# Kernel optimization log

Measured on AMD Instinct MI355X. Metric: run time of the kernel, lower is better.

## Reference

```python
import jax
import jax.numpy as jnp
import numpy as np
from jax import lax

# D dags, L topological levels, K nodes per level, P predecessors per node,
# F = atom/hidden feature dim (104 in original), C = num classes (500)
D, L, K, P, F, C = 256, 64, 64, 8, 104, 500


def setup_inputs() -> dict:
    key = jax.random.key(0)
    ks = jax.random.split(key, 10)
    atom_feats = jax.random.normal(ks[0], (D, L, K, F), dtype=jnp.float32)
    pred_idx = jax.random.randint(ks[1], (D, L - 1, K, P), 0, K, dtype=jnp.int32)
    W1 = jax.random.normal(ks[2], (F, F), dtype=jnp.float32) * 0.1
    b1 = jnp.zeros((F,), dtype=jnp.float32)
    Wm = jax.random.normal(ks[3], (2 * F, F), dtype=jnp.float32) * 0.1
    bm = jnp.zeros((F,), dtype=jnp.float32)
    att_w = jax.random.uniform(ks[4], (F,), dtype=jnp.float32)  # torch.rand init
    dag_w = jax.random.uniform(ks[5], (F,), dtype=jnp.float32)
    Wf = jax.random.normal(ks[6], (F, C), dtype=jnp.float32) * 0.1
    bf = jnp.zeros((C,), dtype=jnp.float32)
    return {"atom_feats": atom_feats, "pred_idx": pred_idx, "W1": W1, "b1": b1,
            "Wm": Wm, "bm": bm, "att_w": att_w, "dag_w": dag_w, "Wf": Wf, "bf": bf}


def reference(atom_feats, pred_idx, W1, b1, Wm, bm, att_w, dag_w, Wf, bf):
    # Level 0: source nodes -> ReLU(NN_single_node(atom))
    out0 = jax.nn.relu(atom_feats[:, 0] @ W1 + b1)  # [D, K, F]

    def step(prev, xs):
        atoms, idx = xs  # atoms [D,K,F], idx [D,K,P]
        # gather predecessor outputs from previous topological level
        preds = jax.vmap(lambda p, i: p[i])(prev, idx)  # [D,K,P,F]
        # softmax attention over the predecessor (stack) axis, elementwise in F
        attn = jax.nn.softmax(att_w * preds, axis=2)
        agg = jnp.sum(attn * preds, axis=2)  # [D,K,F]
        # cat((aggregated, atom)) -> merge -> ReLU
        out = jax.nn.relu(jnp.concatenate([agg, atoms], axis=-1) @ Wm + bm)
        return out, None

    xs = (jnp.swapaxes(atom_feats[:, 1:], 0, 1),  # [L-1, D, K, F]
          jnp.swapaxes(pred_idx, 0, 1))           # [L-1, D, K, P]
    last, _ = lax.scan(step, out0, xs)
    # 'last' output per DAG = last node in topological order
    sink = last[:, -1]  # [D, F]
    # softmax attention over DAG axis with dag_weight, then final linear
    dag_attn = jax.nn.softmax(dag_w * sink, axis=0)
    pooled = jnp.sum(dag_attn * sink, axis=0)  # [F]
    return pooled @ Wf + bf  # [C]
```

## Files before the change

### kernel.cpp

```cpp
#include <hip/hip_runtime.h>
#include <cstddef>

#define Dn 256
#define Ln 64
#define Kn 64
#define Pn 8
#define Fn 104
#define Cn 500
#define KF 6656
#define TPB 896
#define PSTR 108
#define XROWB 512
#define NQ 1664

typedef __attribute__((ext_vector_type(8))) short bh8;
typedef __attribute__((ext_vector_type(4))) float f32x4;

__device__ __forceinline__ unsigned short f2bf_rne(float x) {
  unsigned u = __builtin_bit_cast(unsigned, x);
  u = (u + 0x7fffu + ((u >> 16) & 1u)) >> 16;
  return (unsigned short)u;
}
__device__ __forceinline__ float bf2f(unsigned short h) {
  unsigned u = ((unsigned)h) << 16;
  return __builtin_bit_cast(float, u);
}
__device__ __forceinline__ unsigned pkhi(float a, float b) {
  return __builtin_amdgcn_perm(__builtin_bit_cast(unsigned, b),
                               __builtin_bit_cast(unsigned, a), 0x07060302u);
}
__device__ __forceinline__ float hi_of(float x) {
  return __builtin_bit_cast(float, __builtin_bit_cast(unsigned, x) & 0xffff0000u);
}

__device__ __forceinline__ void stage_quad(char* XAc, char* XBc, int k, int c0,
                                           float v0, float v1, float v2, float v3) {
  uint2 hv, lv;
  hv.x = pkhi(v0, v1); hv.y = pkhi(v2, v3);
  const float r0 = v0 - hi_of(v0), r1 = v1 - hi_of(v1);
  const float r2 = v2 - hi_of(v2), r3 = v3 - hi_of(v3);
  lv.x = pkhi(r0, r1); lv.y = pkhi(r2, r3);
  const int off = k * XROWB + ((((c0 >> 3) ^ (k & 7)) << 4) | ((c0 & 7) << 1));
  *reinterpret_cast<uint2*>(XAc + off) = hv;
  *reinterpret_cast<uint2*>(XBc + off) = lv;
}

__device__ __forceinline__ void load_w_frags(const float* __restrict__ Wg, int Krows,
                                             int col, int e, bh8* Wh, bh8* Wl) {
  #pragma unroll
  for (int kt = 0; kt < 7; ++kt) {
    bh8 h, l;
    #pragma unroll
    for (int v = 0; v < 8; ++v) {
      int k = kt * 32 + e * 8 + v;
      float x = (k < Krows && col < Fn) ? Wg[k * Fn + col] : 0.f;
      unsigned short hh = f2bf_rne(x);
      unsigned short ll = f2bf_rne(x - bf2f(hh));
      h[v] = (short)hh; l[v] = (short)ll;
    }
    Wh[kt] = h; Wl[kt] = l;
  }
}

__device__ __forceinline__ void mfma_gemm(const char* XAc, const char* XBc,
                                          const bh8* Wh, const bh8* Wl,
                                          const float* bms, float* PREVs,
                                          int lane, int col, int mh) {
  const int e = lane >> 4;
  const int rb = lane & 15;
  const float bias = (col < Fn) ? bms[col] : 0.f;
  f32x4 acc[2];
  #pragma unroll
  for (int mti = 0; mti < 2; ++mti) { f32x4 b4 = {bias, bias, bias, bias}; acc[mti] = b4; }
  #pragma unroll
  for (int kt = 0; kt < 7; ++kt) {
    #pragma unroll
    for (int mti = 0; mti < 2; ++mti) {
      const int r = (mh * 2 + mti) * 16 + rb;
      const int chunk = (kt * 4 + e) ^ (rb & 7);
      const bh8 ah = *reinterpret_cast<const bh8*>(XAc + r * XROWB + chunk * 16);
      const bh8 al = *reinterpret_cast<const bh8*>(XBc + r * XROWB + chunk * 16);
      acc[mti] = __builtin_amdgcn_mfma_f32_16x16x32_bf16(ah, Wh[kt], acc[mti], 0, 0, 0);
      acc[mti] = __builtin_amdgcn_mfma_f32_16x16x32_bf16(al, Wh[kt], acc[mti], 0, 0, 0);
      acc[mti] = __builtin_amdgcn_mfma_f32_16x16x32_bf16(ah, Wl[kt], acc[mti], 0, 0, 0);
      acc[mti] = __builtin_amdgcn_mfma_f32_16x16x32_bf16(al, Wl[kt], acc[mti], 0, 0, 0);
    }
  }
  if (col < Fn) {
    #pragma unroll
    for (int mti = 0; mti < 2; ++mti) {
      #pragma unroll
      for (int j = 0; j < 4; ++j) {
        int r = (mh * 2 + mti) * 16 + e * 4 + j;
        PREVs[r * PSTR + col] = fmaxf(acc[mti][j], 0.f);
      }
    }
  }
}

__global__ __launch_bounds__(TPB) void scan_kernel(
    const float* __restrict__ af,
    const int*   __restrict__ pidx,
    const float* __restrict__ W1, const float* __restrict__ b1,
    const float* __restrict__ Wm, const float* __restrict__ bm,
    const float* __restrict__ att_w,
    float* __restrict__ sink)
{
  extern __shared__ char smem[];
  char*  XAc   = smem;
  char*  XBc   = smem + 32768;
  float* PREVs = (float*)(smem + 65536);
  float* bms   = (float*)(smem + 65536 + 27648);
  float* aws   = (float*)(smem + 65536 + 27648 + 448);
  int*   idxs  = (int*)  (smem + 65536 + 27648 + 448 + 416);

  const int t = threadIdx.x;
  const int d = blockIdx.x;
  const int lane = t & 63;
  const int wv = t >> 6;
  const int nt = wv % 7;
  const int mh = wv / 7;
  const int e = lane >> 4;
  const int col = nt * 16 + (lane & 15);

  const float*  afd = af + (size_t)d * (Ln * KF);
  const float4* af4 = reinterpret_cast<const float4*>(afd);
  const int*    pid = pidx + (size_t)d * ((Ln - 1) * Kn * Pn);

  bh8 Wh[7], Wl[7];
  float4 pf4[2];
  int ir0 = 0;

  for (int i = t; i < 16384; i += TPB) reinterpret_cast<unsigned*>(XAc)[i] = 0u;
  if (t < Fn) { bms[t] = b1[t]; aws[t] = att_w[t]; }
  else if (t < 112) bms[t] = 0.f;
  load_w_frags(W1, Fn, col, e, Wh, Wl);
  #pragma unroll
  for (int j = 0; j < 2; ++j) {
    int q = t + j * TPB;
    if (q < NQ) {
      int k = q / 26, fq = (q - k * 26) << 2;
      float4 v = af4[q];
      stage_quad(XAc, XBc, k, fq, v.x, v.y, v.z, v.w);
    }
  }
  __syncthreads();

  mfma_gemm(XAc, XBc, Wh, Wl, bms, PREVs, lane, col, mh);
  __syncthreads();

  load_w_frags(Wm, 2 * Fn, col, e, Wh, Wl);
  if (t < Fn) bms[t] = bm[t];
  if (t < 512) idxs[t] = pid[t];
  #pragma unroll
  for (int j = 0; j < 2; ++j) {
    int q = t + j * TPB;
    if (q < NQ) pf4[j] = af4[NQ + q];
  }
  __syncthreads();

  for (int l = 1; l < Ln; ++l) {
    #pragma unroll
    for (int j = 0; j < 2; ++j) {
      int q = t + j * TPB;
      if (q < NQ) {
        int k = q / 26, fq = (q - k * 26) << 2;
        float4 v = pf4[j];
        stage_quad(XAc, XBc, k, Fn + fq, v.x, v.y, v.z, v.w);
      }
    }
    if (l < 63) {
      const float4* an = af4 + (size_t)(l + 1) * NQ;
      #pragma unroll
      for (int j = 0; j < 2; ++j) {
        int q = t + j * TPB;
        if (q < NQ) pf4[j] = an[q];
      }
      if (t < 512) ir0 = pid[(size_t)l * 512 + t];
    }
    for (int q = t; q < NQ; q += TPB) {
      int k = q / 26, fq = (q - k * 26) << 2;
      const float4 w4 = *reinterpret_cast<const float4*>(aws + fq);
      const float wa[4] = {w4.x, w4.y, w4.z, w4.w};
      const int4 ia = *reinterpret_cast<const int4*>(idxs + (k << 3));
      const int4 ib = *reinterpret_cast<const int4*>(idxs + (k << 3) + 4);
      const int ip[8] = {ia.x, ia.y, ia.z, ia.w, ib.x, ib.y, ib.z, ib.w};
      float vv[8][4];
      #pragma unroll
      for (int p = 0; p < Pn; ++p) {
        float4 v4 = *reinterpret_cast<const float4*>(PREVs + ip[p] * PSTR + fq);
        vv[p][0] = v4.x; vv[p][1] = v4.y; vv[p][2] = v4.z; vv[p][3] = v4.w;
      }
      float ag[4];
      #pragma unroll
      for (int c = 0; c < 4; ++c) {
        float vmax = vv[0][c];
        #pragma unroll
        for (int p = 1; p < Pn; ++p) vmax = fmaxf(vmax, vv[p][c]);
        const float m = wa[c] * vmax;
        float es = 0.f, ps = 0.f;
        #pragma unroll
        for (int p = 0; p < Pn; ++p) {
          float ex = __expf(fmaf(wa[c], vv[p][c], -m));
          es += ex; ps += ex * vv[p][c];
        }
        ag[c] = ps * __builtin_amdgcn_rcpf(es);
      }
      stage_quad(XAc, XBc, k, fq, ag[0], ag[1], ag[2], ag[3]);
    }
    __syncthreads();

    mfma_gemm(XAc, XBc, Wh, Wl, bms, PREVs, lane, col, mh);
    if (l < 63 && t < 512) idxs[t] = ir0;
    __syncthreads();
  }

  if (t < Fn) sink[d * Fn + t] = PREVs[(Kn - 1) * PSTR + t];
}

__global__ __launch_bounds__(512) void final_kernel(
    const float* __restrict__ sink, const float* __restrict__ dag_w,
    const float* __restrict__ Wf, const float* __restrict__ bf,
    float* __restrict__ out)
{
  extern __shared__ char smem[];
  float* ss = (float*)smem;
  float* pooled = ss + Dn * Fn;
  const int t = threadIdx.x;
  for (int i = t; i < Dn * Fn; i += 512) ss[i] = sink[i];
  __syncthreads();
  if (t < Fn) {
    float wvv = dag_w[t];
    float m = -3.0e38f;
    for (int dd = 0; dd < Dn; ++dd) m = fmaxf(m, wvv * ss[dd * Fn + t]);
    float es = 0.f, ps = 0.f;
    for (int dd = 0; dd < Dn; ++dd) {
      float v = ss[dd * Fn + t];
      float ex = __expf(wvv * v - m);
      es += ex; ps += ex * v;
    }
    pooled[t] = ps / es;
  }
  __syncthreads();
  if (t < Cn) {
    float a = bf[t];
    for (int f = 0; f < Fn; ++f) a = fmaf(pooled[f], Wf[f * Cn + t], a);
    out[t] = a;
  }
}

extern "C" void kernel_launch(void* const* d_in, const int* in_sizes, int n_in,
                              void* d_out, int out_size, void* d_ws, size_t ws_size,
                              hipStream_t stream) {
  const float* af    = (const float*)d_in[0];
  const int*   pidx  = (const int*)  d_in[1];
  const float* W1    = (const float*)d_in[2];
  const float* b1    = (const float*)d_in[3];
  const float* Wm    = (const float*)d_in[4];
  const float* bm    = (const float*)d_in[5];
  const float* att_w = (const float*)d_in[6];
  const float* dag_w = (const float*)d_in[7];
  const float* Wf    = (const float*)d_in[8];
  const float* bf    = (const float*)d_in[9];
  float* out  = (float*)d_out;
  float* sink = (float*)d_ws;

  constexpr size_t SMEM1 = 96096;
  constexpr size_t SMEM2 = (size_t)(Dn * Fn + Fn) * 4;

  (void)hipFuncSetAttribute((const void*)scan_kernel,
                      hipFuncAttributeMaxDynamicSharedMemorySize, (int)SMEM1);
  (void)hipFuncSetAttribute((const void*)final_kernel,
                      hipFuncAttributeMaxDynamicSharedMemorySize, (int)SMEM2);

  scan_kernel<<<Dn, TPB, SMEM1, stream>>>(af, pidx, W1, b1, Wm, bm, att_w, sink);
  final_kernel<<<1, 512, SMEM2, stream>>>(sink, dag_w, Wf, bf, out);
}
```

Before: 364.3 us.

## Overlap atom-half GEMM with attention aggregation and trim split-bf16 MFMAs

Swaps the concat order so atom features occupy the first K-tiles, letting the atom part of the merge GEMM run before the predecessor softmax aggregation and only the aggregated part runs after the barrier. Drops the lo*lo MFMA term of the split-bf16 emulation, cutting a quarter of MFMA work at some accuracy cost. Softmax uses exp2 with att_w pre-scaled by log2(e), and packed f32 FMA/add/mul for the elementwise math. Adds an extra barrier per level and keeps the accumulators live across the aggregation phase, which raises register pressure.

```diff
diff --git a/kernel.cpp b/kernel.cpp
--- a/kernel.cpp
+++ b/kernel.cpp
@@ -1,5 +1,6 @@
 #include <hip/hip_runtime.h>
 #include <cstddef>
+#include <math.h>
 
 #define Dn 256
 #define Ln 64
@@ -15,6 +16,19 @@
 
 typedef __attribute__((ext_vector_type(8))) short bh8;
 typedef __attribute__((ext_vector_type(4))) float f32x4;
+typedef __attribute__((ext_vector_type(2))) float f32x2;
+
+__device__ __forceinline__ f32x2 pk_fma(f32x2 a, f32x2 b, f32x2 c) {
+  f32x2 d;
+  asm("v_pk_fma_f32 %0, %1, %2, %3" : "=v"(d) : "v"(a), "v"(b), "v"(c));
+  return d;
+}
+__device__ __forceinline__ f32x2 pk_add(f32x2 a, f32x2 b) {
+  f32x2 d; asm("v_pk_add_f32 %0, %1, %2" : "=v"(d) : "v"(a), "v"(b)); return d;
+}
+__device__ __forceinline__ f32x2 pk_mul(f32x2 a, f32x2 b) {
+  f32x2 d; asm("v_pk_mul_f32 %0, %1, %2" : "=v"(d) : "v"(a), "v"(b)); return d;
+}
 
 __device__ __forceinline__ unsigned short f2bf_rne(float x) {
   unsigned u = __builtin_bit_cast(unsigned, x);
@@ -62,18 +76,33 @@
   }
 }
 
-__device__ __forceinline__ void mfma_gemm(const char* XAc, const char* XBc,
+__device__ __forceinline__ void load_w_frags_swapped(const float* __restrict__ Wg,
+                                                     int col, int e, bh8* Wh, bh8* Wl) {
+  #pragma unroll
+  for (int kt = 0; kt < 7; ++kt) {
+    bh8 h, l;
+    #pragma unroll
+    for (int v = 0; v < 8; ++v) {
+      int k = kt * 32 + e * 8 + v;
+      int row = (k < Fn) ? (k + Fn) : (k < 2 * Fn ? k - Fn : -1);
+      float x = (row >= 0 && col < Fn) ? Wg[row * Fn + col] : 0.f;
+      unsigned short hh = f2bf_rne(x);
+      unsigned short ll = f2bf_rne(x - bf2f(hh));
+      h[v] = (short)hh; l[v] = (short)ll;
+    }
+    Wh[kt] = h; Wl[kt] = l;
+  }
+}
+
+__device__ __forceinline__ void gemm_part(const char* XAc, const char* XBc,
                                           const bh8* Wh, const bh8* Wl,
-                                          const float* bms, float* PREVs,
-                                          int lane, int col, int mh) {
+                                          f32x4 acc[2], int lane, int mh,
+                                          int k0, int k1) {
   const int e = lane >> 4;
   const int rb = lane & 15;
-  const float bias = (col < Fn) ? bms[col] : 0.f;
-  f32x4 acc[2];
-  #pragma unroll
-  for (int mti = 0; mti < 2; ++mti) { f32x4 b4 = {bias, bias, bias, bias}; acc[mti] = b4; }
   #pragma unroll
   for (int kt = 0; kt < 7; ++kt) {
+    if (kt < k0 || kt >= k1) continue;
     #pragma unroll
     for (int mti = 0; mti < 2; ++mti) {
       const int r = (mh * 2 + mti) * 16 + rb;
@@ -83,9 +112,13 @@
       acc[mti] = __builtin_amdgcn_mfma_f32_16x16x32_bf16(ah, Wh[kt], acc[mti], 0, 0, 0);
       acc[mti] = __builtin_amdgcn_mfma_f32_16x16x32_bf16(al, Wh[kt], acc[mti], 0, 0, 0);
       acc[mti] = __builtin_amdgcn_mfma_f32_16x16x32_bf16(ah, Wl[kt], acc[mti], 0, 0, 0);
-      acc[mti] = __builtin_amdgcn_mfma_f32_16x16x32_bf16(al, Wl[kt], acc[mti], 0, 0, 0);
-    }
-  }
+    }
+  }
+}
+
+__device__ __forceinline__ void gemm_epilogue(f32x4 acc[2], float* PREVs,
+                                              int lane, int col, int mh) {
+  const int e = lane >> 4;
   if (col < Fn) {
     #pragma unroll
     for (int mti = 0; mti < 2; ++mti) {
@@ -117,9 +150,9 @@
   const int t = threadIdx.x;
   const int d = blockIdx.x;
   const int lane = t & 63;
-  const int wv = t >> 6;
-  const int nt = wv % 7;
-  const int mh = wv / 7;
+  const int wvi = t >> 6;
+  const int nt = wvi % 7;
+  const int mh = wvi / 7;
   const int e = lane >> 4;
   const int col = nt * 16 + (lane & 15);
 
@@ -132,7 +165,7 @@
   int ir0 = 0;
 
   for (int i = t; i < 16384; i += TPB) reinterpret_cast<unsigned*>(XAc)[i] = 0u;
-  if (t < Fn) { bms[t] = b1[t]; aws[t] = att_w[t]; }
+  if (t < Fn) { bms[t] = b1[t]; aws[t] = att_w[t] * 1.44269504f; }
   else if (t < 112) bms[t] = 0.f;
   load_w_frags(W1, Fn, col, e, Wh, Wl);
   #pragma unroll
@@ -146,10 +179,17 @@
   }
   __syncthreads();
 
-  mfma_gemm(XAc, XBc, Wh, Wl, bms, PREVs, lane, col, mh);
-  __syncthreads();
-
-  load_w_frags(Wm, 2 * Fn, col, e, Wh, Wl);
+  {
+    const float bias = (col < Fn) ? bms[col] : 0.f;
+    f32x4 acc[2];
+    #pragma unroll
+    for (int mti = 0; mti < 2; ++mti) { f32x4 b4 = {bias, bias, bias, bias}; acc[mti] = b4; }
+    gemm_part(XAc, XBc, Wh, Wl, acc, lane, mh, 0, 4);
+    gemm_epilogue(acc, PREVs, lane, col, mh);
+  }
+  __syncthreads();
+
+  load_w_frags_swapped(Wm, col, e, Wh, Wl);
   if (t < Fn) bms[t] = bm[t];
   if (t < 512) idxs[t] = pid[t];
   #pragma unroll
@@ -166,7 +206,7 @@
       if (q < NQ) {
         int k = q / 26, fq = (q - k * 26) << 2;
         float4 v = pf4[j];
-        stage_quad(XAc, XBc, k, Fn + fq, v.x, v.y, v.z, v.w);
+        stage_quad(XAc, XBc, k, fq, v.x, v.y, v.z, v.w);
       }
     }
     if (l < 63) {
@@ -178,39 +218,66 @@
       }
       if (t < 512) ir0 = pid[(size_t)l * 512 + t];
     }
+    __syncthreads();
+
+    const float bias = (col < Fn) ? bms[col] : 0.f;
+    f32x4 acc[2];
+    #pragma unroll
+    for (int mti = 0; mti < 2; ++mti) { f32x4 b4 = {bias, bias, bias, bias}; acc[mti] = b4; }
+    gemm_part(XAc, XBc, Wh, Wl, acc, lane, mh, 0, 3);
+
     for (int q = t; q < NQ; q += TPB) {
       int k = q / 26, fq = (q - k * 26) << 2;
       const float4 w4 = *reinterpret_cast<const float4*>(aws + fq);
-      const float wa[4] = {w4.x, w4.y, w4.z, w4.w};
+      const f32x2 wa01 = {w4.x, w4.y}, wa23 = {w4.z, w4.w};
       const int4 ia = *reinterpret_cast<const int4*>(idxs + (k << 3));
       const int4 ib = *reinterpret_cast<const int4*>(idxs + (k << 3) + 4);
       const int ip[8] = {ia.x, ia.y, ia.z, ia.w, ib.x, ib.y, ib.z, ib.w};
-      float vv[8][4];
+      float4 vvp[8];
+      #pragma unroll
+      for (int p = 0; p < Pn; ++p)
+        vvp[p] = *reinterpret_cast<const float4*>(PREVs + ip[p] * PSTR + fq);
+      float m0, m1, m2, m3;
+      m0 = fmaxf(fmaxf(vvp[0].x, vvp[1].x), vvp[2].x);
+      m0 = fmaxf(fmaxf(m0, vvp[3].x), vvp[4].x);
+      m0 = fmaxf(fmaxf(m0, vvp[5].x), vvp[6].x);
+      m0 = fmaxf(m0, vvp[7].x);
+      m1 = fmaxf(fmaxf(vvp[0].y, vvp[1].y), vvp[2].y);
+      m1 = fmaxf(fmaxf(m1, vvp[3].y), vvp[4].y);
+      m1 = fmaxf(fmaxf(m1, vvp[5].y), vvp[6].y);
+      m1 = fmaxf(m1, vvp[7].y);
+      m2 = fmaxf(fmaxf(vvp[0].z, vvp[1].z), vvp[2].z);
+      m2 = fmaxf(fmaxf(m2, vvp[3].z), vvp[4].z);
+      m2 = fmaxf(fmaxf(m2, vvp[5].z), vvp[6].z);
+      m2 = fmaxf(m2, vvp[7].z);
+      m3 = fmaxf(fmaxf(vvp[0].w, vvp[1].w), vvp[2].w);
+      m3 = fmaxf(fmaxf(m3, vvp[3].w), vvp[4].w);
+      m3 = fmaxf(fmaxf(m3, vvp[5].w), vvp[6].w);
+      m3 = fmaxf(m3, vvp[7].w);
+      const f32x2 mm01 = {-m0, -m1}, mm23 = {-m2, -m3};
+      const f32x2 nm01 = pk_mul(wa01, mm01), nm23 = pk_mul(wa23, mm23);
+      f32x2 es01 = {0.f, 0.f}, es23 = {0.f, 0.f};
+      f32x2 ps01 = {0.f, 0.f}, ps23 = {0.f, 0.f};
       #pragma unroll
       for (int p = 0; p < Pn; ++p) {
-        float4 v4 = *reinterpret_cast<const float4*>(PREVs + ip[p] * PSTR + fq);
-        vv[p][0] = v4.x; vv[p][1] = v4.y; vv[p][2] = v4.z; vv[p][3] = v4.w;
+        const f32x2 v01 = {vvp[p].x, vvp[p].y}, v23 = {vvp[p].z, vvp[p].w};
+        const f32x2 a01 = pk_fma(wa01, v01, nm01);
+        const f32x2 a23 = pk_fma(wa23, v23, nm23);
+        const f32x2 e01 = {exp2f(a01.x), exp2f(a01.y)};
+        const f32x2 e23 = {exp2f(a23.x), exp2f(a23.y)};
+        es01 = pk_add(es01, e01); es23 = pk_add(es23, e23);
+        ps01 = pk_fma(e01, v01, ps01); ps23 = pk_fma(e23, v23, ps23);
       }
-      float ag[4];
-      #pragma unroll
-      for (int c = 0; c < 4; ++c) {
-        float vmax = vv[0][c];
-        #pragma unroll
-        for (int p = 1; p < Pn; ++p) vmax = fmaxf(vmax, vv[p][c]);
-        const float m = wa[c] * vmax;
-        float es = 0.f, ps = 0.f;
-        #pragma unroll
-        for (int p = 0; p < Pn; ++p) {
-          float ex = __expf(fmaf(wa[c], vv[p][c], -m));
-          es += ex; ps += ex * vv[p][c];
-        }
-        ag[c] = ps * __builtin_amdgcn_rcpf(es);
-      }
-      stage_quad(XAc, XBc, k, fq, ag[0], ag[1], ag[2], ag[3]);
+      const float ag0 = ps01.x * __builtin_amdgcn_rcpf(es01.x);
+      const float ag1 = ps01.y * __builtin_amdgcn_rcpf(es01.y);
+      const float ag2 = ps23.x * __builtin_amdgcn_rcpf(es23.x);
+      const float ag3 = ps23.y * __builtin_amdgcn_rcpf(es23.y);
+      stage_quad(XAc, XBc, k, Fn + fq, ag0, ag1, ag2, ag3);
     }
     __syncthreads();
 
-    mfma_gemm(XAc, XBc, Wh, Wl, bms, PREVs, lane, col, mh);
+    gemm_part(XAc, XBc, Wh, Wl, acc, lane, mh, 3, 7);
+    gemm_epilogue(acc, PREVs, lane, col, mh);
     if (l < 63 && t < 512) idxs[t] = ir0;
     __syncthreads();
   }
```

Result: slower. 599.2 us (+64.5%).
